# Kernel tuning notes

Measured on AMD Instinct MI355X. Metric: run time of the kernel, lower is better.

Reference implementation:

```python
import jax, jax.numpy as jnp
import numpy as np

NUM_HEADS = 8
CHUNK = 64          # dialtion / chunck_size
EPS = 1e-5          # InstanceNorm1d eps
NEG = -1e9


def setup_inputs() -> dict:
    key = jax.random.key(0)
    ks = jax.random.split(key, 8)
    N, C, T = 4, 512, 4096
    x = jax.random.normal(ks[0], (N, C, T), dtype=jnp.float32)
    q = jax.random.normal(ks[1], (N, C, T), dtype=jnp.float32)
    k = jax.random.normal(ks[2], (N, C, T), dtype=jnp.float32)
    v = jax.random.normal(ks[3], (N, C, T), dtype=jnp.float32)
    masks = jnp.ones((N, 1, T), dtype=jnp.float32)
    s = 1.0 / np.sqrt(C)
    W_in = jax.random.normal(ks[4], (3 * C, C), dtype=jnp.float32) * s   # packed q/k/v in-proj
    b_in = jnp.zeros((3 * C,), dtype=jnp.float32)
    W_out = jax.random.normal(ks[5], (C, C), dtype=jnp.float32) * s     # out-proj
    b_out = jnp.zeros((C,), dtype=jnp.float32)
    return {"x": x, "q": q, "k": k, "v": v, "masks": masks,
            "W_in": W_in, "b_in": b_in, "W_out": W_out, "b_out": b_out}


def _chunk_attn(q, k, v, masks, W_in, b_in, W_out, b_out):
    # q,k,v: [N, C, T]; masks: [N, 1, T]
    N, C, T = q.shape
    H, Dh = NUM_HEADS, C // NUM_HEADS
    nc = T // CHUNK
    Wq, Wk, Wv = jnp.split(W_in, 3, axis=0)
    bq, bk, bv = jnp.split(b_in, 3, axis=0)

    def proj(t, W, b):
        # [N,C,T] -> chunked heads [N, nc, CHUNK, H, Dh]
        t = t.transpose(0, 2, 1) @ W.T + b            # [N, T, C]
        return t.reshape(N, nc, CHUNK, H, Dh)

    qh = proj(q, Wq, bq)
    kh = proj(k, Wk, bk)
    vh = proj(v, Wv, bv)

    scale = 1.0 / jnp.sqrt(jnp.asarray(Dh, q.dtype))
    # intra-chunk scores: [N, nc, H, CHUNK, CHUNK]
    scores = jnp.einsum('bnqhd,bnkhd->bnhqk', qh, kh) * scale
    km = masks[:, 0, :].reshape(N, nc, CHUNK)         # key validity per chunk
    scores = scores + jnp.where(km[:, :, None, None, :] > 0, 0.0, NEG)
    attn = jax.nn.softmax(scores, axis=-1)
    out = jnp.einsum('bnhqk,bnkhd->bnqhd', attn, vh).reshape(N, T, C)
    out = out @ W_out.T + b_out                        # [N, T, C]
    out = out.transpose(0, 2, 1) * masks               # [N, C, T], re-mask
    return out


def reference(x, q, k, v, masks, W_in, b_in, W_out, b_out):
    out = _chunk_attn(q, k, v, masks, W_in, b_in, W_out, b_out) + x
    # InstanceNorm1d (affine=False): normalize each (n, c) row over T
    mu = jnp.mean(out, axis=2, keepdims=True)
    var = jnp.mean(jnp.square(out - mu), axis=2, keepdims=True)
    return (out - mu) * jax.lax.rsqrt(var + EPS)
```

## Files before the change

kernel.cpp:

```cpp
#include <hip/hip_runtime.h>
#include <hip/hip_bf16.h>

#define NB 4
#define CC 512
#define TT 4096
#define C3 1536
#define CQK 1024
#define NTC (NB*TT*CC)

typedef __attribute__((ext_vector_type(4))) float f32x4;
typedef __attribute__((ext_vector_type(8))) short short8;
typedef unsigned short ushort;

__device__ __forceinline__ ushort f2bf(float f){
    union { float f; unsigned u; } x; x.f = f;
    unsigned r = x.u + 0x7fffu + ((x.u >> 16) & 1u);
    return (ushort)(r >> 16);
}

__device__ __forceinline__ void gload16(const void* g, void* l){
    __builtin_amdgcn_global_load_lds((const __attribute__((address_space(1))) void*)g,
                                     (__attribute__((address_space(3))) void*)l,
                                     16, 0, 0);
}

__global__ __launch_bounds__(256) void cvt_w(const float* __restrict__ Wi,
                                             const float* __restrict__ Wo,
                                             ushort* __restrict__ Wb,
                                             ushort* __restrict__ Wob){
    int t = blockIdx.x * 256 + threadIdx.x;
    const float* src; ushort* dst; int idx;
    if (t < 196608){ src = Wi; dst = Wb;  idx = t; }
    else           { src = Wo; dst = Wob; idx = t - 196608; }
    f32x4 v = *((const f32x4*)src + idx);
    ushort4 o;
    o.x = f2bf(v[0]); o.y = f2bf(v[1]); o.z = f2bf(v[2]); o.w = f2bf(v[3]);
    *((ushort4*)dst + idx) = o;
}

__global__ __launch_bounds__(256) void transpose_cvt(const float* __restrict__ q,
                                                     const float* __restrict__ k,
                                                     const float* __restrict__ v,
                                                     ushort* __restrict__ XT){
    __shared__ float sT[64][65];
    int b = blockIdx.x;
    int tch = b % 64;  b /= 64;
    int cch = b % 8;   b /= 8;
    int n   = b % 4;   b /= 4;
    int which = b;
    const float* src = (which == 0) ? q : (which == 1) ? k : v;
    const float* base = src + (size_t)n*CC*TT + (size_t)(cch*64)*TT + (size_t)tch*64;
    for (int i = 0; i < 4; ++i){
        int f = i*256 + threadIdx.x;
        int t4 = f & 15, c = f >> 4;
        f32x4 val = *(const f32x4*)(base + (size_t)c*TT + t4*4);
        for (int j = 0; j < 4; ++j) sT[t4*4 + j][c] = val[j];
    }
    __syncthreads();
    ushort* dst = XT + (size_t)which*NTC + ((size_t)n*TT + (size_t)tch*64)*CC + cch*64;
    for (int i = 0; i < 4; ++i){
        int f = i*256 + threadIdx.x;
        int c4 = f & 15, t = f >> 4;
        ushort4 o;
        o.x = f2bf(sT[t][c4*4+0]); o.y = f2bf(sT[t][c4*4+1]);
        o.z = f2bf(sT[t][c4*4+2]); o.w = f2bf(sT[t][c4*4+3]);
        *(ushort4*)(dst + (size_t)t*CC + c4*4) = o;
    }
}

__global__ __launch_bounds__(256) void proj_gemm(const ushort* __restrict__ XT,
                                                 const ushort* __restrict__ Wb,
                                                 const float* __restrict__ b_in,
                                                 ushort* __restrict__ P,
                                                 ushort* __restrict__ Vt){
    __shared__ ushort sA[128*64];
    __shared__ ushort sB[128*64];
    const int tid = threadIdx.x;
    const int bid = blockIdx.x;
    const int mtile  = ((bid & 7) << 4) | ((bid >> 3) & 15);
    const int cotile = bid >> 7;
    const int co0 = cotile * 128;
    const int m0  = mtile * 128;
    const int which = co0 >> 9;
    const ushort* Abase = XT + (size_t)which*NTC + (size_t)m0*CC;
    const ushort* Bbase = Wb + (size_t)co0*CC;
    const int w = tid >> 6, lane = tid & 63;
    const int wr = w >> 1, wc = w & 1;
    const int l15 = lane & 15, quad = lane >> 4;

    const ushort* gA[4]; const ushort* gB[4];
    ushort* lA[4]; ushort* lB[4];
    for (int i = 0; i < 4; ++i){
        int slot = i*256 + tid;
        int m = slot >> 3, k8 = slot & 7, kk = k8 ^ (m & 7);
        gA[i] = Abase + (size_t)m*CC + kk*8;
        gB[i] = Bbase + (size_t)m*CC + kk*8;
        int lbase = (i*256 + (tid & ~63)) * 8;
        lA[i] = sA + lbase;  lB[i] = sB + lbase;
    }

    f32x4 acc[4][4] = {};
    for (int kb = 0; kb < 8; ++kb){
        __syncthreads();
        for (int i = 0; i < 4; ++i){
            gload16(gA[i] + kb*64, lA[i]);
            gload16(gB[i] + kb*64, lB[i]);
        }
        __syncthreads();
        for (int ks = 0; ks < 2; ++ks){
            short8 aF[4], bF[4];
            for (int mi = 0; mi < 4; ++mi){
                int m = wr*64 + mi*16 + l15;
                aF[mi] = *(const short8*)&sA[(m*8 + ((ks*4 + quad) ^ (m & 7)))*8];
            }
            for (int ni = 0; ni < 4; ++ni){
                int m = wc*64 + ni*16 + l15;
                bF[ni] = *(const short8*)&sB[(m*8 + ((ks*4 + quad) ^ (m & 7)))*8];
            }
            for (int mi = 0; mi < 4; ++mi)
                for (int ni = 0; ni < 4; ++ni)
                    acc[mi][ni] = __builtin_amdgcn_mfma_f32_16x16x32_bf16(
                        aF[mi], bF[ni], acc[mi][ni], 0, 0, 0);
        }
    }

    float bj[4];
    for (int ni = 0; ni < 4; ++ni) bj[ni] = b_in[co0 + wc*64 + ni*16 + l15];
    if (which < 2){
        for (int mi = 0; mi < 4; ++mi){
            int m = m0 + wr*64 + mi*16 + quad*4;
            for (int ni = 0; ni < 4; ++ni){
                int col = (co0 & 511) + wc*64 + ni*16 + l15;
                ushort* dst = P + (size_t)m*CQK + which*512 + col;
                for (int r = 0; r < 4; ++r)
                    dst[(size_t)r*CQK] = f2bf(acc[mi][ni][r] + bj[ni]);
            }
        }
    } else {
        for (int mi = 0; mi < 4; ++mi){
            int m = m0 + wr*64 + mi*16 + quad*4;
            int n = m >> 12, t = m & 4095;
            for (int ni = 0; ni < 4; ++ni){
                int col = (co0 & 511) + wc*64 + ni*16 + l15;
                int h = col >> 6, d = col & 63;
                ushort4 o4;
                o4.x = f2bf(acc[mi][ni][0] + bj[ni]);
                o4.y = f2bf(acc[mi][ni][1] + bj[ni]);
                o4.z = f2bf(acc[mi][ni][2] + bj[ni]);
                o4.w = f2bf(acc[mi][ni][3] + bj[ni]);
                *(ushort4*)&Vt[(((size_t)n*8 + h)*64 + d)*TT + t] = o4;
            }
        }
    }
}

__global__ __launch_bounds__(256) void attn_kernel(const ushort* __restrict__ P,
                                                   const ushort* __restrict__ Vt,
                                                   const float* __restrict__ masks,
                                                   ushort* __restrict__ ctx){
    __shared__ ushort sQ[64*64], sK[64*64], sV[64*64];
    __shared__ ushort sP[64][72];
    int bid = blockIdx.x;
    int h = bid & 7, ch = (bid >> 3) & 63, n = bid >> 9;
    const int tid = threadIdx.x, lane = tid & 63, w = tid >> 6;
    const int l15 = lane & 15, quad = lane >> 4;
    const size_t rowbase = (size_t)n*TT + (size_t)ch*64;
    for (int i = 0; i < 2; ++i){
        int slot = i*256 + tid;
        int r = slot >> 3, k8 = slot & 7, kk = k8 ^ (r & 7);
        int lbase = (i*256 + (tid & ~63)) * 8;
        const ushort* gq = P + (rowbase + r)*CQK + h*64 + kk*8;
        gload16(gq,        sQ + lbase);
        gload16(gq + 512,  sK + lbase);
        const ushort* gv = Vt + (((size_t)n*8 + h)*64 + r)*TT + ch*64 + kk*8;
        gload16(gv,        sV + lbase);
    }
    __syncthreads();
    const int m0w = w*16;
    short8 aQ[2]; f32x4 accS[4] = {};
    for (int ks = 0; ks < 2; ++ks){
        int m = m0w + l15;
        aQ[ks] = *(const short8*)&sQ[(m*8 + ((ks*4 + quad) ^ (m & 7)))*8];
    }
    for (int ni = 0; ni < 4; ++ni)
        for (int ks = 0; ks < 2; ++ks){
            int m = ni*16 + l15;
            short8 bK = *(const short8*)&sK[(m*8 + ((ks*4 + quad) ^ (m & 7)))*8];
            accS[ni] = __builtin_amdgcn_mfma_f32_16x16x32_bf16(aQ[ks], bK, accS[ni], 0,0,0);
        }
    float madd[4];
    for (int ni = 0; ni < 4; ++ni){
        float mv = masks[(size_t)n*TT + ch*64 + ni*16 + l15];
        madd[ni] = (mv > 0.f) ? 0.f : -1e9f;
    }
    float s[4][4];
    for (int ni = 0; ni < 4; ++ni)
        for (int r = 0; r < 4; ++r) s[ni][r] = accS[ni][r]*0.125f + madd[ni];
    float ex[4][4];
    for (int r = 0; r < 4; ++r){
        float m1 = fmaxf(fmaxf(s[0][r], s[1][r]), fmaxf(s[2][r], s[3][r]));
        for (int d = 1; d < 16; d <<= 1) m1 = fmaxf(m1, __shfl_xor(m1, d));
        float a = 0.f;
        for (int ni = 0; ni < 4; ++ni){ float e = __expf(s[ni][r] - m1); ex[ni][r] = e; a += e; }
        for (int d = 1; d < 16; d <<= 1) a += __shfl_xor(a, d);
        float rs = 1.0f / a;
        for (int ni = 0; ni < 4; ++ni)
            sP[m0w + quad*4 + r][ni*16 + l15] = f2bf(ex[ni][r] * rs);
    }
    short8 aP[2]; f32x4 accO[4] = {};
    for (int ks = 0; ks < 2; ++ks)
        aP[ks] = *(const short8*)&sP[m0w + l15][ks*32 + quad*8];
    for (int ni = 0; ni < 4; ++ni)
        for (int ks = 0; ks < 2; ++ks){
            int m = ni*16 + l15;
            short8 bV = *(const short8*)&sV[(m*8 + ((ks*4 + quad) ^ (m & 7)))*8];
            accO[ni] = __builtin_amdgcn_mfma_f32_16x16x32_bf16(aP[ks], bV, accO[ni], 0,0,0);
        }
    for (int ni = 0; ni < 4; ++ni)
        for (int r = 0; r < 4; ++r){
            size_t row = rowbase + m0w + quad*4 + r;
            ctx[row*CC + h*64 + ni*16 + l15] = f2bf(accO[ni][r]);
        }
}

__global__ __launch_bounds__(256) void out_gemm(const ushort* __restrict__ ctx,
                                                const ushort* __restrict__ Wob,
                                                const float* __restrict__ b_out,
                                                const float* __restrict__ x,
                                                const float* __restrict__ masks,
                                                float* __restrict__ out){
    __shared__ ushort sA[128*64];
    __shared__ ushort sB[128*64];
    const int tid = threadIdx.x;
    const int bid = blockIdx.x;
    const int mtile  = ((bid & 7) << 4) | ((bid >> 3) & 15);
    const int cotile = bid >> 7;
    const int co0 = cotile * 128;
    const int m0  = mtile * 128;
    const int n = m0 >> 12, t0 = m0 & 4095;
    const ushort* Abase = ctx + (size_t)m0*CC;
    const ushort* Bbase = Wob + (size_t)co0*CC;
    const int w = tid >> 6, lane = tid & 63;
    const int wr = w >> 1, wc = w & 1;
    const int l15 = lane & 15, quad = lane >> 4;

    const ushort* gA[4]; const ushort* gB[4];
    ushort* lA[4]; ushort* lB[4];
    for (int i = 0; i < 4; ++i){
        int slot = i*256 + tid;
        int m = slot >> 3, k8 = slot & 7, kk = k8 ^ (m & 7);
        gA[i] = Abase + (size_t)m*CC + kk*8;
        gB[i] = Bbase + (size_t)m*CC + kk*8;
        int lbase = (i*256 + (tid & ~63)) * 8;
        lA[i] = sA + lbase;  lB[i] = sB + lbase;
    }

    f32x4 acc[4][4] = {};
    for (int kb = 0; kb < 8; ++kb){
        __syncthreads();
        for (int i = 0; i < 4; ++i){
            gload16(gA[i] + kb*64, lA[i]);
            gload16(gB[i] + kb*64, lB[i]);
        }
        __syncthreads();
        for (int ks = 0; ks < 2; ++ks){
            short8 aF[4], bF[4];
            for (int mi = 0; mi < 4; ++mi){
                int m = wr*64 + mi*16 + l15;
                aF[mi] = *(const short8*)&sA[(m*8 + ((ks*4 + quad) ^ (m & 7)))*8];
            }
            for (int ni = 0; ni < 4; ++ni){
                int m = wc*64 + ni*16 + l15;
                bF[ni] = *(const short8*)&sB[(m*8 + ((ks*4 + quad) ^ (m & 7)))*8];
            }
            for (int mi = 0; mi < 4; ++mi)
                for (int ni = 0; ni < 4; ++ni)
                    acc[mi][ni] = __builtin_amdgcn_mfma_f32_16x16x32_bf16(
                        aF[mi], bF[ni], acc[mi][ni], 0, 0, 0);
        }
    }
    float bo[4];
    for (int ni = 0; ni < 4; ++ni) bo[ni] = b_out[co0 + wc*64 + ni*16 + l15];
    for (int mi = 0; mi < 4; ++mi){
        int t = t0 + wr*64 + mi*16 + quad*4;
        f32x4 mk = *(const f32x4*)(masks + (size_t)n*TT + t);
        for (int ni = 0; ni < 4; ++ni){
            int co = co0 + wc*64 + ni*16 + l15;
            const f32x4 xv = *(const f32x4*)(x + ((size_t)n*CC + co)*TT + t);
            f32x4 o;
            for (int r = 0; r < 4; ++r)
                o[r] = (acc[mi][ni][r] + bo[ni]) * mk[r] + xv[r];
            *(f32x4*)(out + ((size_t)n*CC + co)*TT + t) = o;
        }
    }
}

__global__ __launch_bounds__(256) void inorm(float* __restrict__ out){
    __shared__ float sS[4], sQ2[4];
    float* row = out + (size_t)blockIdx.x * TT;
    f32x4 vbuf[4];
    float s = 0.f, ss = 0.f;
    for (int i = 0; i < 4; ++i){
        f32x4 vv = *(const f32x4*)(row + (size_t)(i*256 + threadIdx.x)*4);
        vbuf[i] = vv;
        for (int r = 0; r < 4; ++r){ s += vv[r]; ss += vv[r]*vv[r]; }
    }
    for (int d = 1; d < 64; d <<= 1){ s += __shfl_xor(s, d); ss += __shfl_xor(ss, d); }
    int w = threadIdx.x >> 6;
    if ((threadIdx.x & 63) == 0){ sS[w] = s; sQ2[w] = ss; }
    __syncthreads();
    s  = sS[0] + sS[1] + sS[2] + sS[3];
    ss = sQ2[0] + sQ2[1] + sQ2[2] + sQ2[3];
    float mean = s * (1.0f/TT);
    float var  = ss * (1.0f/TT) - mean*mean;
    float rstd = rsqrtf(var + 1e-5f);
    for (int i = 0; i < 4; ++i){
        f32x4 vv = vbuf[i], o;
        for (int r = 0; r < 4; ++r) o[r] = (vv[r] - mean) * rstd;
        *(f32x4*)(row + (size_t)(i*256 + threadIdx.x)*4) = o;
    }
}

extern "C" void kernel_launch(void* const* d_in, const int* in_sizes, int n_in,
                              void* d_out, int out_size, void* d_ws, size_t ws_size,
                              hipStream_t stream) {
    const float* x     = (const float*)d_in[0];
    const float* q     = (const float*)d_in[1];
    const float* k     = (const float*)d_in[2];
    const float* v     = (const float*)d_in[3];
    const float* masks = (const float*)d_in[4];
    const float* W_in  = (const float*)d_in[5];
    const float* b_in  = (const float*)d_in[6];
    const float* W_out = (const float*)d_in[7];
    const float* b_out = (const float*)d_in[8];
    float* out = (float*)d_out;

    ushort* ws  = (ushort*)d_ws;
    ushort* XT  = ws;
    ushort* Wb  = ws + (size_t)3*NTC;
    ushort* Wob = Wb + 786432;
    ushort* P   = Wob + 262144;
    ushort* Vt  = P + (size_t)NB*TT*CQK;
    ushort* ctx = ws;

    cvt_w<<<1024, 256, 0, stream>>>(W_in, W_out, Wb, Wob);
    transpose_cvt<<<6144, 256, 0, stream>>>(q, k, v, XT);
    proj_gemm<<<1536, 256, 0, stream>>>(XT, Wb, b_in, P, Vt);
    attn_kernel<<<2048, 256, 0, stream>>>(P, Vt, masks, ctx);
    out_gemm<<<512, 256, 0, stream>>>(ctx, Wob, b_out, x, masks, out);
    inorm<<<2048, 256, 0, stream>>>(out);
}
```

Measured before the change: 269.1 us.

## Merge weight conversion into transpose kernel and halve out-GEMM column tile

Fuses the weight fp32-to-bf16 conversion and the q/k/v transpose-convert into one prep launch. Each transpose block now handles four 64-step time tiles, prefetching the next tile's loads into registers while the current one goes through shared memory. The output GEMM tile shrinks from 128x128 to 128x64, doubling the grid from 512 to 1024 blocks to fill more compute units. The cost is fewer blocks in prep, extra synchronisation per tile, and less operand reuse per block in the output GEMM.

```diff
diff --git a/kernel.cpp b/kernel.cpp
--- a/kernel.cpp
+++ b/kernel.cpp
@@ -24,47 +24,64 @@
                                      16, 0, 0);
 }
 
-__global__ __launch_bounds__(256) void cvt_w(const float* __restrict__ Wi,
-                                             const float* __restrict__ Wo,
-                                             ushort* __restrict__ Wb,
-                                             ushort* __restrict__ Wob){
-    int t = blockIdx.x * 256 + threadIdx.x;
-    const float* src; ushort* dst; int idx;
-    if (t < 196608){ src = Wi; dst = Wb;  idx = t; }
-    else           { src = Wo; dst = Wob; idx = t - 196608; }
-    f32x4 v = *((const f32x4*)src + idx);
-    ushort4 o;
-    o.x = f2bf(v[0]); o.y = f2bf(v[1]); o.z = f2bf(v[2]); o.w = f2bf(v[3]);
-    *((ushort4*)dst + idx) = o;
-}
-
-__global__ __launch_bounds__(256) void transpose_cvt(const float* __restrict__ q,
-                                                     const float* __restrict__ k,
-                                                     const float* __restrict__ v,
-                                                     ushort* __restrict__ XT){
+__global__ __launch_bounds__(256) void prep(const float* __restrict__ q,
+                                            const float* __restrict__ k,
+                                            const float* __restrict__ v,
+                                            const float* __restrict__ Wi,
+                                            const float* __restrict__ Wo,
+                                            ushort* __restrict__ XT,
+                                            ushort* __restrict__ Wb,
+                                            ushort* __restrict__ Wob){
     __shared__ float sT[64][65];
+    const int tid = threadIdx.x;
     int b = blockIdx.x;
-    int tch = b % 64;  b /= 64;
-    int cch = b % 8;   b /= 8;
-    int n   = b % 4;   b /= 4;
+    if (b >= 1536){
+        int idx0 = (b - 1536) * 1024 + tid;
+        for (int i = 0; i < 4; ++i){
+            int idx = idx0 + i*256;
+            const float* src; ushort* dst; int j;
+            if (idx < 196608){ src = Wi; dst = Wb;  j = idx; }
+            else             { src = Wo; dst = Wob; j = idx - 196608; }
+            f32x4 vv = *((const f32x4*)src + j);
+            ushort4 o;
+            o.x = f2bf(vv[0]); o.y = f2bf(vv[1]); o.z = f2bf(vv[2]); o.w = f2bf(vv[3]);
+            *((ushort4*)dst + j) = o;
+        }
+        return;
+    }
+    int tq = b & 15;  b >>= 4;
+    int cch = b & 7;  b >>= 3;
+    int n   = b & 3;  b >>= 2;
     int which = b;
     const float* src = (which == 0) ? q : (which == 1) ? k : v;
-    const float* base = src + (size_t)n*CC*TT + (size_t)(cch*64)*TT + (size_t)tch*64;
-    for (int i = 0; i < 4; ++i){
-        int f = i*256 + threadIdx.x;
-        int t4 = f & 15, c = f >> 4;
-        f32x4 val = *(const f32x4*)(base + (size_t)c*TT + t4*4);
-        for (int j = 0; j < 4; ++j) sT[t4*4 + j][c] = val[j];
-    }
-    __syncthreads();
-    ushort* dst = XT + (size_t)which*NTC + ((size_t)n*TT + (size_t)tch*64)*CC + cch*64;
-    for (int i = 0; i < 4; ++i){
-        int f = i*256 + threadIdx.x;
-        int c4 = f & 15, t = f >> 4;
-        ushort4 o;
-        o.x = f2bf(sT[t][c4*4+0]); o.y = f2bf(sT[t][c4*4+1]);
-        o.z = f2bf(sT[t][c4*4+2]); o.w = f2bf(sT[t][c4*4+3]);
-        *(ushort4*)(dst + (size_t)t*CC + c4*4) = o;
+    const float* base = src + (size_t)n*CC*TT + (size_t)(cch*64)*TT + (size_t)tq*256;
+    ushort* dstb = XT + (size_t)which*NTC + ((size_t)n*TT + (size_t)tq*256)*CC + cch*64;
+
+    int t4l[4], cl[4];
+    for (int i = 0; i < 4; ++i){ int f = i*256 + tid; t4l[i] = f & 15; cl[i] = f >> 4; }
+
+    f32x4 cur[4], nxt[4];
+    for (int i = 0; i < 4; ++i)
+        cur[i] = *(const f32x4*)(base + (size_t)cl[i]*TT + t4l[i]*4);
+    #pragma unroll
+    for (int s = 0; s < 4; ++s){
+        if (s < 3)
+            for (int i = 0; i < 4; ++i)
+                nxt[i] = *(const f32x4*)(base + (size_t)cl[i]*TT + (s+1)*64 + t4l[i]*4);
+        for (int i = 0; i < 4; ++i)
+            for (int j = 0; j < 4; ++j) sT[t4l[i]*4 + j][cl[i]] = cur[i][j];
+        __syncthreads();
+        ushort* dst = dstb + (size_t)(s*64)*CC;
+        for (int i = 0; i < 4; ++i){
+            int f = i*256 + tid;
+            int c4 = f & 15, t = f >> 4;
+            ushort4 o;
+            o.x = f2bf(sT[t][c4*4+0]); o.y = f2bf(sT[t][c4*4+1]);
+            o.z = f2bf(sT[t][c4*4+2]); o.w = f2bf(sT[t][c4*4+3]);
+            *(ushort4*)(dst + (size_t)t*CC + c4*4) = o;
+        }
+        __syncthreads();
+        for (int i = 0; i < 4; ++i) cur[i] = nxt[i];
     }
 }
 
@@ -230,12 +247,12 @@
                                                 const float* __restrict__ masks,
                                                 float* __restrict__ out){
     __shared__ ushort sA[128*64];
-    __shared__ ushort sB[128*64];
+    __shared__ ushort sB[64*64];
     const int tid = threadIdx.x;
     const int bid = blockIdx.x;
     const int mtile  = ((bid & 7) << 4) | ((bid >> 3) & 15);
     const int cotile = bid >> 7;
-    const int co0 = cotile * 128;
+    const int co0 = cotile * 64;
     const int m0  = mtile * 128;
     const int n = m0 >> 12, t0 = m0 & 4095;
     const ushort* Abase = ctx + (size_t)m0*CC;
@@ -244,48 +261,50 @@
     const int wr = w >> 1, wc = w & 1;
     const int l15 = lane & 15, quad = lane >> 4;
 
-    const ushort* gA[4]; const ushort* gB[4];
-    ushort* lA[4]; ushort* lB[4];
+    const ushort* gA[4]; ushort* lA[4];
+    const ushort* gB[2]; ushort* lB[2];
     for (int i = 0; i < 4; ++i){
         int slot = i*256 + tid;
         int m = slot >> 3, k8 = slot & 7, kk = k8 ^ (m & 7);
         gA[i] = Abase + (size_t)m*CC + kk*8;
+        lA[i] = sA + (i*256 + (tid & ~63)) * 8;
+    }
+    for (int i = 0; i < 2; ++i){
+        int slot = i*256 + tid;
+        int m = slot >> 3, k8 = slot & 7, kk = k8 ^ (m & 7);
         gB[i] = Bbase + (size_t)m*CC + kk*8;
-        int lbase = (i*256 + (tid & ~63)) * 8;
-        lA[i] = sA + lbase;  lB[i] = sB + lbase;
-    }
-
-    f32x4 acc[4][4] = {};
+        lB[i] = sB + (i*256 + (tid & ~63)) * 8;
+    }
+
+    f32x4 acc[4][2] = {};
     for (int kb = 0; kb < 8; ++kb){
         __syncthreads();
-        for (int i = 0; i < 4; ++i){
-            gload16(gA[i] + kb*64, lA[i]);
-            gload16(gB[i] + kb*64, lB[i]);
-        }
+        for (int i = 0; i < 4; ++i) gload16(gA[i] + kb*64, lA[i]);
+        for (int i = 0; i < 2; ++i) gload16(gB[i] + kb*64, lB[i]);
         __syncthreads();
         for (int ks = 0; ks < 2; ++ks){
-            short8 aF[4], bF[4];
+            short8 aF[4], bF[2];
             for (int mi = 0; mi < 4; ++mi){
                 int m = wr*64 + mi*16 + l15;
                 aF[mi] = *(const short8*)&sA[(m*8 + ((ks*4 + quad) ^ (m & 7)))*8];
             }
-            for (int ni = 0; ni < 4; ++ni){
-                int m = wc*64 + ni*16 + l15;
+            for (int ni = 0; ni < 2; ++ni){
+                int m = wc*32 + ni*16 + l15;
                 bF[ni] = *(const short8*)&sB[(m*8 + ((ks*4 + quad) ^ (m & 7)))*8];
             }
             for (int mi = 0; mi < 4; ++mi)
-                for (int ni = 0; ni < 4; ++ni)
+                for (int ni = 0; ni < 2; ++ni)
                     acc[mi][ni] = __builtin_amdgcn_mfma_f32_16x16x32_bf16(
                         aF[mi], bF[ni], acc[mi][ni], 0, 0, 0);
         }
     }
-    float bo[4];
-    for (int ni = 0; ni < 4; ++ni) bo[ni] = b_out[co0 + wc*64 + ni*16 + l15];
+    float bo[2];
+    for (int ni = 0; ni < 2; ++ni) bo[ni] = b_out[co0 + wc*32 + ni*16 + l15];
     for (int mi = 0; mi < 4; ++mi){
         int t = t0 + wr*64 + mi*16 + quad*4;
         f32x4 mk = *(const f32x4*)(masks + (size_t)n*TT + t);
-        for (int ni = 0; ni < 4; ++ni){
-            int co = co0 + wc*64 + ni*16 + l15;
+        for (int ni = 0; ni < 2; ++ni){
+            int co = co0 + wc*32 + ni*16 + l15;
             const f32x4 xv = *(const f32x4*)(x + ((size_t)n*CC + co)*TT + t);
             f32x4 o;
             for (int r = 0; r < 4; ++r)
@@ -343,10 +362,9 @@
     ushort* Vt  = P + (size_t)NB*TT*CQK;
     ushort* ctx = ws;
 
-    cvt_w<<<1024, 256, 0, stream>>>(W_in, W_out, Wb, Wob);
-    transpose_cvt<<<6144, 256, 0, stream>>>(q, k, v, XT);
+    prep<<<1792, 256, 0, stream>>>(q, k, v, W_in, W_out, XT, Wb, Wob);
     proj_gemm<<<1536, 256, 0, stream>>>(XT, Wb, b_in, P, Vt);
     attn_kernel<<<2048, 256, 0, stream>>>(P, Vt, masks, ctx);
-    out_gemm<<<512, 256, 0, stream>>>(ctx, Wob, b_out, x, masks, out);
+    out_gemm<<<1024, 256, 0, stream>>>(ctx, Wob, b_out, x, masks, out);
     inorm<<<2048, 256, 0, stream>>>(out);
 }
```

After: 261.4 us. 1.03x faster.
